# Optimization experiments

Measured on AMD Instinct MI355X. Metric: run time of the kernel, lower is better.

## Reference

```python
import jax, jax.numpy as jnp
import numpy as np

B, H, D, K, V, M = 64, 32, 4096, 128, 128, 4095

def setup_inputs() -> dict:
    key = jax.random.key(0)
    ks = jax.random.split(key, 7)
    return {
        "x": jax.random.normal(ks[0], (B, D), dtype=jnp.float32),
        "prev_K": jax.random.normal(ks[1], (B, M, K), dtype=jnp.float32),
        "prev_V": jax.random.normal(ks[2], (B, M, V), dtype=jnp.float32),
        "Wq": jax.random.normal(ks[3], (H, D, K), dtype=jnp.float32),
        "Wk": jax.random.normal(ks[4], (D, K), dtype=jnp.float32),
        "Wv": jax.random.normal(ks[5], (D, V), dtype=jnp.float32),
        "Wo": jax.random.normal(ks[6], (H, V, D), dtype=jnp.float32),
    }

def reference(x, prev_K, prev_V, Wq, Wk, Wv, Wo):
    # Projections
    q = jnp.einsum('bd,hdk->bhk', x, Wq)            # [b,h,k]
    k_new = jnp.einsum('bd,dk->bk', x, Wk)          # [b,k]
    v_new = jnp.einsum('bd,dv->bv', x, Wv)          # [b,v]
    Kc = jnp.concatenate([prev_K, k_new[:, None, :]], axis=1)  # [b,m+1,k]
    Vc = jnp.concatenate([prev_V, v_new[:, None, :]], axis=1)  # [b,m+1,v]
    # Shared-KV attention (MQA)
    logits = jnp.einsum('bhk,bmk->bhm', q, Kc)
    weights = jax.nn.softmax(logits, axis=-1)
    o = jnp.einsum('bhm,bmv->bhv', weights, Vc)
    y = jnp.einsum('bhv,hvd->bd', o, Wo)
    return (y, Kc, Vc)
```

## Files before the change

kernel.cpp:

```cpp
#include <hip/hip_runtime.h>
#include <stdint.h>

#define B_  64
#define H_  32
#define D_  4096
#define KD  128
#define VD  128
#define M_  4095
#define M1_ 4096
#define NCHUNK 32
#define LOG2E 1.44269504088896f

#define WS_P      0ull
#define WS_Q      4456448ull
#define WS_STATS  4718592ull
#define WS_O      4849664ull
#define WS_OPART  5111808ull

#define WAITVL(n) asm volatile("s_waitcnt vmcnt(" #n ") lgkmcnt(0)" ::: "memory")
#define WAITL()  asm volatile("s_waitcnt lgkmcnt(0)" ::: "memory")
#define BAR()    __builtin_amdgcn_s_barrier()

typedef __attribute__((address_space(3))) char lds_char;
typedef const __attribute__((address_space(1))) char glb_char;

__global__ __launch_bounds__(256) void k_proj_partial(
    const float* __restrict__ x, const float* __restrict__ Wq,
    const float* __restrict__ Wk, const float* __restrict__ Wv,
    float* __restrict__ P) {
  __shared__ float xs[64][260];
  const int dc = blockIdx.x;
  const int hx = blockIdx.y;
  const int t  = threadIdx.x;
  const float* xsrc = x + dc * 256;
  #pragma unroll
  for (int j = 0; j < 16; ++j) {
    int f = t + 256 * j;
    int row = f >> 6, c4 = f & 63;
    *(float4*)&xs[row][c4 * 4] =
        *(const float4*)(xsrc + (size_t)row * D_ + c4 * 4);
  }
  __syncthreads();
  const int bq = t >> 4;
  const int kg = t & 15;
  const int b0 = bq * 4;
  const float* W = (hx < H_) ? (Wq + (size_t)hx * D_ * KD)
                             : ((hx == H_) ? Wk : Wv);
  const float* wp = W + (size_t)(dc * 256) * KD + kg * 8;
  float acc[4][8];
  #pragma unroll
  for (int i = 0; i < 4; ++i)
    #pragma unroll
    for (int j = 0; j < 8; ++j) acc[i][j] = 0.f;
  #pragma unroll 8
  for (int d = 0; d < 256; ++d) {
    float4 w0 = *(const float4*)(wp + (size_t)d * KD);
    float4 w1 = *(const float4*)(wp + (size_t)d * KD + 4);
    float xv[4];
    #pragma unroll
    for (int i = 0; i < 4; ++i) xv[i] = xs[b0 + i][d];
    #pragma unroll
    for (int i = 0; i < 4; ++i) {
      acc[i][0] += xv[i] * w0.x; acc[i][1] += xv[i] * w0.y;
      acc[i][2] += xv[i] * w0.z; acc[i][3] += xv[i] * w0.w;
      acc[i][4] += xv[i] * w1.x; acc[i][5] += xv[i] * w1.y;
      acc[i][6] += xv[i] * w1.z; acc[i][7] += xv[i] * w1.w;
    }
  }
  #pragma unroll
  for (int i = 0; i < 4; ++i) {
    size_t base = ((size_t)(dc * 64 + b0 + i) * 34 + hx) * KD + kg * 8;
    *(float4*)&P[base]     = make_float4(acc[i][0], acc[i][1], acc[i][2], acc[i][3]);
    *(float4*)&P[base + 4] = make_float4(acc[i][4], acc[i][5], acc[i][6], acc[i][7]);
  }
}

__global__ __launch_bounds__(256) void k_proj_reduce(
    const float* __restrict__ P, float* __restrict__ q,
    float* __restrict__ Kc, float* __restrict__ Vc) {
  int i = blockIdx.x * 256 + threadIdx.x;
  int k = i & 127;
  int hx = (i >> 7) % 34;
  int b = i / (128 * 34);
  float s = 0.f;
  #pragma unroll
  for (int dc = 0; dc < 16; ++dc)
    s += P[(size_t)dc * (64 * 34 * 128) + (size_t)(b * 34 + hx) * 128 + k];
  if (hx < H_)       q[((size_t)b * H_ + hx) * KD + k] = s;
  else if (hx == H_) Kc[((size_t)b * M1_ + M_) * KD + k] = s;
  else               Vc[((size_t)b * M1_ + M_) * VD + k] = s;
}

__device__ __forceinline__ void stage_issue(
    const float* src, const float* app_row, float* lbuf, int m_lo, int t) {
  const int wb = t & ~63;
  #pragma unroll
  for (int j = 0; j < 4; ++j) {
    int f = j * 256 + t;
    int r = f >> 5, p = f & 31;
    int m = m_lo + r;
    int g4 = p ^ (r & 7);
    const float* gp = (m < M_) ? (src + (size_t)m * 128 + g4 * 4)
                               : (app_row + g4 * 4);
    __builtin_amdgcn_global_load_lds(
        (glb_char*)gp, (lds_char*)(lbuf + (size_t)(j * 256 + wb) * 4),
        16, 0, 0);
  }
}

__device__ __forceinline__ void copy_out(
    const float* lbuf, float* dst, int m_lo, int t) {
  const int r = t >> 3;
  const int m = m_lo + r;
  float* drow = dst + (size_t)m * 128;
  #pragma unroll
  for (int jj = 0; jj < 4; ++jj) {
    int g4 = (t & 7) + jj * 8;
    int p = g4 ^ (r & 7);
    float4 v = *(const float4*)&lbuf[(r * 32 + p) * 4];
    *(float4*)(drow + g4 * 4) = v;
  }
}

__global__ __launch_bounds__(256, 3) void k_flash(
    const float* __restrict__ prevK, const float* __restrict__ prevV,
    const float* __restrict__ q, float* __restrict__ Kc, float* __restrict__ Vc,
    float* __restrict__ o_part, float* __restrict__ stats) {
  __shared__ float buf[2][32 * 128];
  __shared__ float upool[4608];
  const int chunk = blockIdx.x;
  const int b = blockIdx.y;
  const int t = threadIdx.x;
  const int m0 = chunk * 128;

  const float* kbase = prevK + (size_t)b * M_ * KD;
  const float* vbase = prevV + (size_t)b * M_ * VD;
  const float* kapp  = Kc + ((size_t)b * M1_ + M_) * KD;
  const float* vapp  = Vc + ((size_t)b * M1_ + M_) * VD;
  float* kc = Kc + (size_t)b * M1_ * KD;
  float* vc = Vc + (size_t)b * M1_ * VD;

  const float* qsrc = q + (size_t)b * H_ * KD;
  float4 qv4[4];
  #pragma unroll
  for (int j = 0; j < 4; ++j) {
    int f = j * 256 + t;
    qv4[j] = *(const float4*)(qsrc + (size_t)(f >> 5) * KD + (f & 31) * 4);
  }
  stage_issue(kbase, kapp, buf[0], m0, t);
  #pragma unroll
  for (int j = 0; j < 4; ++j) {
    int f = j * 256 + t;
    *(float4*)&upool[(f >> 5) * 132 + (f & 31) * 4] = qv4[j];
  }

  const int mg = t & 15, hg = t >> 4, h0 = hg * 2;
  const int v4 = t & 31, hoct = t >> 5, h0v = hoct * 4;

  float accL0[8], accL1[8];

#define LOGITS_TILE(S, BUFI)                                                  \
  {                                                                           \
    const float* lb = buf[BUFI];                                              \
    float c00 = 0.f, c01 = 0.f, c10 = 0.f, c11 = 0.f;                         \
    const int sw = (mg & 7);                                                  \
    _Pragma("unroll 4")                                                       \
    for (int k4 = 0; k4 < 32; ++k4) {                                         \
      int p = (k4 ^ sw) * 4;                                                  \
      float4 qa = *(const float4*)&upool[h0 * 132 + k4 * 4];                  \
      float4 qb = *(const float4*)&upool[(h0 + 1) * 132 + k4 * 4];            \
      float4 k0v = *(const float4*)&lb[mg * 128 + p];                         \
      float4 k1v = *(const float4*)&lb[(mg + 16) * 128 + p];                  \
      c00 += qa.x*k0v.x + qa.y*k0v.y + qa.z*k0v.z + qa.w*k0v.w;               \
      c01 += qa.x*k1v.x + qa.y*k1v.y + qa.z*k1v.z + qa.w*k1v.w;               \
      c10 += qb.x*k0v.x + qb.y*k0v.y + qb.z*k0v.z + qb.w*k0v.w;               \
      c11 += qb.x*k1v.x + qb.y*k1v.y + qb.z*k1v.z + qb.w*k1v.w;               \
    }                                                                         \
    accL0[(S) * 2]     = c00;                                                 \
    accL0[(S) * 2 + 1] = c01;                                                 \
    accL1[(S) * 2]     = c10;                                                 \
    accL1[(S) * 2 + 1] = c11;                                                 \
  }

#define PV_TILE(S, BUFI)                                                      \
  {                                                                           \
    const float* lb = buf[BUFI];                                              \
    _Pragma("unroll 4")                                                       \
    for (int mm = 0; mm < 32; ++mm) {                                         \
      int p = (v4 ^ (mm & 7)) * 4;                                            \
      float4 gv = *(const float4*)&lb[mm * 128 + p];                          \
      float4 w4 = *(const float4*)&upool[((S) * 32 + mm) * 36 + h0v];         \
      a0.x += w4.x*gv.x; a0.y += w4.x*gv.y; a0.z += w4.x*gv.z; a0.w += w4.x*gv.w; \
      a1.x += w4.y*gv.x; a1.y += w4.y*gv.y; a1.z += w4.y*gv.z; a1.w += w4.y*gv.w; \
      a2.x += w4.z*gv.x; a2.y += w4.z*gv.y; a2.z += w4.z*gv.z; a2.w += w4.z*gv.w; \
      a3.x += w4.w*gv.x; a3.y += w4.w*gv.y; a3.z += w4.w*gv.z; a3.w += w4.w*gv.w; \
    }                                                                         \
  }

  stage_issue(kbase, kapp, buf[1], m0 + 32, t);
  WAITVL(4); BAR();
  LOGITS_TILE(0, 0);
  copy_out(buf[0], kc, m0, t);
  WAITL(); BAR();

  stage_issue(kbase, kapp, buf[0], m0 + 64, t);
  WAITVL(8); BAR();
  LOGITS_TILE(1, 1);
  copy_out(buf[1], kc, m0 + 32, t);
  WAITL(); BAR();

  stage_issue(kbase, kapp, buf[1], m0 + 96, t);
  WAITVL(8); BAR();
  LOGITS_TILE(2, 0);
  copy_out(buf[0], kc, m0 + 64, t);
  WAITL(); BAR();

  stage_issue(vbase, vapp, buf[0], m0, t);
  WAITVL(8); BAR();
  LOGITS_TILE(3, 1);
  copy_out(buf[1], kc, m0 + 96, t);
  WAITL(); BAR();

  {
    float mx0 = -3.402823466e38f, mx1 = -3.402823466e38f;
    #pragma unroll
    for (int j = 0; j < 8; ++j) {
      mx0 = fmaxf(mx0, accL0[j]);
      mx1 = fmaxf(mx1, accL1[j]);
    }
    #pragma unroll
    for (int off = 1; off <= 8; off <<= 1) {
      mx0 = fmaxf(mx0, __shfl_xor(mx0, off));
      mx1 = fmaxf(mx1, __shfl_xor(mx1, off));
    }
    float s0 = 0.f, s1 = 0.f;
    #pragma unroll
    for (int j = 0; j < 8; ++j) {
      float e0 = exp2f((accL0[j] - mx0) * LOG2E); accL0[j] = e0; s0 += e0;
      float e1 = exp2f((accL1[j] - mx1) * LOG2E); accL1[j] = e1; s1 += e1;
    }
    #pragma unroll
    for (int off = 1; off <= 8; off <<= 1) {
      s0 += __shfl_xor(s0, off);
      s1 += __shfl_xor(s1, off);
    }
    #pragma unroll
    for (int s = 0; s < 4; ++s)
      #pragma unroll
      for (int i = 0; i < 2; ++i) {
        int m = s * 32 + mg + 16 * i;
        upool[m * 36 + h0]     = accL0[s * 2 + i];
        upool[m * 36 + h0 + 1] = accL1[s * 2 + i];
      }
    if (mg == 0) {
      size_t sb0 = (((size_t)b * H_ + h0) * NCHUNK + chunk) * 2;
      *(float2*)&stats[sb0] = make_float2(mx0, s0);
      size_t sb1 = (((size_t)b * H_ + h0 + 1) * NCHUNK + chunk) * 2;
      *(float2*)&stats[sb1] = make_float2(mx1, s1);
    }
  }
  WAITL(); BAR();

  float4 a0 = {0,0,0,0}, a1 = {0,0,0,0}, a2 = {0,0,0,0}, a3 = {0,0,0,0};

  stage_issue(vbase, vapp, buf[1], m0 + 32, t);
  WAITVL(10); BAR();
  PV_TILE(0, 0);
  copy_out(buf[0], vc, m0, t);
  WAITL(); BAR();

  stage_issue(vbase, vapp, buf[0], m0 + 64, t);
  WAITVL(8); BAR();
  PV_TILE(1, 1);
  copy_out(buf[1], vc, m0 + 32, t);
  WAITL(); BAR();

  stage_issue(vbase, vapp, buf[1], m0 + 96, t);
  WAITVL(8); BAR();
  PV_TILE(2, 0);
  copy_out(buf[0], vc, m0 + 64, t);
  WAITL(); BAR();

  WAITVL(4); BAR();
  PV_TILE(3, 1);
  copy_out(buf[1], vc, m0 + 96, t);

  size_t base = ((size_t)(chunk * B_ + b) * H_ + h0v) * VD + v4 * 4;
  *(float4*)&o_part[base]          = a0;
  *(float4*)&o_part[base + VD]     = a1;
  *(float4*)&o_part[base + 2 * VD] = a2;
  *(float4*)&o_part[base + 3 * VD] = a3;
#undef LOGITS_TILE
#undef PV_TILE
}

__global__ __launch_bounds__(128) void k_combine(
    const float* __restrict__ o_part, const float* __restrict__ stats,
    float* __restrict__ o) {
  const int bh = blockIdx.x;
  const int t = threadIdx.x;
  __shared__ float st[64];
  if (t < 64) st[t] = stats[(size_t)bh * 64 + t];
  __syncthreads();
  float M = -3.402823466e38f;
  #pragma unroll
  for (int c = 0; c < NCHUNK; ++c) M = fmaxf(M, st[2 * c]);
  float wc[NCHUNK];
  float denom = 0.f;
  #pragma unroll
  for (int c = 0; c < NCHUNK; ++c) {
    float e = exp2f((st[2 * c] - M) * LOG2E);
    wc[c] = e;
    denom += st[2 * c + 1] * e;
  }
  const float inv = 1.0f / denom;
  const int b = bh >> 5, h = bh & 31;
  float acc = 0.f;
  #pragma unroll 4
  for (int c = 0; c < NCHUNK; ++c)
    acc += wc[c] * o_part[((size_t)(c * B_ + b) * H_ + h) * VD + t];
  o[(size_t)bh * VD + t] = acc * inv;
}

__global__ __launch_bounds__(256) void k_out_partial(
    const float* __restrict__ o, const float* __restrict__ Wo,
    float* __restrict__ Py) {
  __shared__ float os[64][260];
  const int dc = blockIdx.x;
  const int hvc = blockIdx.y;
  const int t = threadIdx.x;
  #pragma unroll
  for (int j = 0; j < 16; ++j) {
    int f = t + 256 * j;
    int row = f >> 6, c4 = f & 63;
    *(float4*)&os[row][c4 * 4] =
        *(const float4*)(o + (size_t)row * 4096 + hvc * 256 + c4 * 4);
  }
  __syncthreads();
  const int bq = t >> 4, dg = t & 15;
  const int b0 = bq * 4;
  const float* wp = Wo + (size_t)(hvc * 256) * D_ + dc * 128 + dg * 8;
  float acc[4][8];
  #pragma unroll
  for (int i = 0; i < 4; ++i)
    #pragma unroll
    for (int j = 0; j < 8; ++j) acc[i][j] = 0.f;
  #pragma unroll 8
  for (int hv = 0; hv < 256; ++hv) {
    float4 w0 = *(const float4*)(wp + (size_t)hv * D_);
    float4 w1 = *(const float4*)(wp + (size_t)hv * D_ + 4);
    float ov[4];
    #pragma unroll
    for (int i = 0; i < 4; ++i) ov[i] = os[b0 + i][hv];
    #pragma unroll
    for (int i = 0; i < 4; ++i) {
      acc[i][0] += ov[i] * w0.x; acc[i][1] += ov[i] * w0.y;
      acc[i][2] += ov[i] * w0.z; acc[i][3] += ov[i] * w0.w;
      acc[i][4] += ov[i] * w1.x; acc[i][5] += ov[i] * w1.y;
      acc[i][6] += ov[i] * w1.z; acc[i][7] += ov[i] * w1.w;
    }
  }
  #pragma unroll
  for (int i = 0; i < 4; ++i) {
    size_t base = ((size_t)hvc * 64 + b0 + i) * 4096 + dc * 128 + dg * 8;
    *(float4*)&Py[base]     = make_float4(acc[i][0], acc[i][1], acc[i][2], acc[i][3]);
    *(float4*)&Py[base + 4] = make_float4(acc[i][4], acc[i][5], acc[i][6], acc[i][7]);
  }
}

__global__ __launch_bounds__(256) void k_yreduce(
    const float* __restrict__ Py, float* __restrict__ y) {
  int i = blockIdx.x * 256 + threadIdx.x;
  float s = 0.f;
  #pragma unroll
  for (int c = 0; c < 16; ++c) s += Py[(size_t)c * 262144 + i];
  y[i] = s;
}

extern "C" void kernel_launch(void* const* d_in, const int* in_sizes, int n_in,
                              void* d_out, int out_size, void* d_ws, size_t ws_size,
                              hipStream_t stream) {
  const float* x     = (const float*)d_in[0];
  const float* prevK = (const float*)d_in[1];
  const float* prevV = (const float*)d_in[2];
  const float* Wq    = (const float*)d_in[3];
  const float* Wk    = (const float*)d_in[4];
  const float* Wv    = (const float*)d_in[5];
  const float* Wo    = (const float*)d_in[6];

  float* y  = (float*)d_out;
  float* Kc = y + (size_t)B_ * D_;
  float* Vc = Kc + (size_t)B_ * M1_ * KD;

  float* ws     = (float*)d_ws;
  float* P      = ws + WS_P;
  float* q      = ws + WS_Q;
  float* stats  = ws + WS_STATS;
  float* o      = ws + WS_O;
  float* o_part = ws + WS_OPART;

  k_proj_partial<<<dim3(16, 34), 256, 0, stream>>>(x, Wq, Wk, Wv, P);
  k_proj_reduce<<<1088, 256, 0, stream>>>(P, q, Kc, Vc);
  k_flash<<<dim3(32, 64), 256, 0, stream>>>(prevK, prevV, q, Kc, Vc, o_part, stats);
  k_combine<<<2048, 128, 0, stream>>>(o_part, stats, o);
  k_out_partial<<<dim3(32, 16), 256, 0, stream>>>(o, Wo, P);
  k_yreduce<<<1024, 256, 0, stream>>>(P, y);
}
```

Baseline: 262.0 us.

## Read V directly from global in PV loop instead of LDS staging

The PV phase no longer stages V tiles through LDS with async loads and barriers. Each thread now reads V rows straight from global memory, and one wave group writes the Vc copy. The second K stage issue is moved earlier and the V prefetch during the logits phase is dropped. This is meant to cut barrier and LDS traffic, at the cost of redundant global reads across the 8 head groups and less latency hiding.

```diff
diff --git a/kernel.cpp b/kernel.cpp
--- a/kernel.cpp
+++ b/kernel.cpp
@@ -148,6 +148,7 @@
     qv4[j] = *(const float4*)(qsrc + (size_t)(f >> 5) * KD + (f & 31) * 4);
   }
   stage_issue(kbase, kapp, buf[0], m0, t);
+  stage_issue(kbase, kapp, buf[1], m0 + 32, t);
   #pragma unroll
   for (int j = 0; j < 4; ++j) {
     int f = j * 256 + t;
@@ -182,22 +183,6 @@
     accL1[(S) * 2 + 1] = c11;                                                 \
   }
 
-#define PV_TILE(S, BUFI)                                                      \
-  {                                                                           \
-    const float* lb = buf[BUFI];                                              \
-    _Pragma("unroll 4")                                                       \
-    for (int mm = 0; mm < 32; ++mm) {                                         \
-      int p = (v4 ^ (mm & 7)) * 4;                                            \
-      float4 gv = *(const float4*)&lb[mm * 128 + p];                          \
-      float4 w4 = *(const float4*)&upool[((S) * 32 + mm) * 36 + h0v];         \
-      a0.x += w4.x*gv.x; a0.y += w4.x*gv.y; a0.z += w4.x*gv.z; a0.w += w4.x*gv.w; \
-      a1.x += w4.y*gv.x; a1.y += w4.y*gv.y; a1.z += w4.y*gv.z; a1.w += w4.y*gv.w; \
-      a2.x += w4.z*gv.x; a2.y += w4.z*gv.y; a2.z += w4.z*gv.z; a2.w += w4.z*gv.w; \
-      a3.x += w4.w*gv.x; a3.y += w4.w*gv.y; a3.z += w4.w*gv.z; a3.w += w4.w*gv.w; \
-    }                                                                         \
-  }
-
-  stage_issue(kbase, kapp, buf[1], m0 + 32, t);
   WAITVL(4); BAR();
   LOGITS_TILE(0, 0);
   copy_out(buf[0], kc, m0, t);
@@ -213,10 +198,7 @@
   WAITVL(8); BAR();
   LOGITS_TILE(2, 0);
   copy_out(buf[0], kc, m0 + 64, t);
-  WAITL(); BAR();
-
-  stage_issue(vbase, vapp, buf[0], m0, t);
-  WAITVL(8); BAR();
+  WAITVL(4); BAR();
   LOGITS_TILE(3, 1);
   copy_out(buf[1], kc, m0 + 96, t);
   WAITL(); BAR();
@@ -261,37 +243,28 @@
   }
   WAITL(); BAR();
 
-  float4 a0 = {0,0,0,0}, a1 = {0,0,0,0}, a2 = {0,0,0,0}, a3 = {0,0,0,0};
-
-  stage_issue(vbase, vapp, buf[1], m0 + 32, t);
-  WAITVL(10); BAR();
-  PV_TILE(0, 0);
-  copy_out(buf[0], vc, m0, t);
-  WAITL(); BAR();
-
-  stage_issue(vbase, vapp, buf[0], m0 + 64, t);
-  WAITVL(8); BAR();
-  PV_TILE(1, 1);
-  copy_out(buf[1], vc, m0 + 32, t);
-  WAITL(); BAR();
-
-  stage_issue(vbase, vapp, buf[1], m0 + 96, t);
-  WAITVL(8); BAR();
-  PV_TILE(2, 0);
-  copy_out(buf[0], vc, m0 + 64, t);
-  WAITL(); BAR();
-
-  WAITVL(4); BAR();
-  PV_TILE(3, 1);
-  copy_out(buf[1], vc, m0 + 96, t);
-
-  size_t base = ((size_t)(chunk * B_ + b) * H_ + h0v) * VD + v4 * 4;
-  *(float4*)&o_part[base]          = a0;
-  *(float4*)&o_part[base + VD]     = a1;
-  *(float4*)&o_part[base + 2 * VD] = a2;
-  *(float4*)&o_part[base + 3 * VD] = a3;
+  {
+    float4 a0 = {0,0,0,0}, a1 = {0,0,0,0}, a2 = {0,0,0,0}, a3 = {0,0,0,0};
+    #pragma unroll 8
+    for (int mm = 0; mm < 128; ++mm) {
+      const int mv = m0 + mm;
+      const float* vrow = (mv < M_) ? (vbase + (size_t)mv * VD) : vapp;
+      float4 gv = *(const float4*)(vrow + v4 * 4);
+      if (hoct == 0 && mv < M_)
+        *(float4*)(vc + (size_t)mv * VD + v4 * 4) = gv;
+      float4 w4 = *(const float4*)&upool[mm * 36 + h0v];
+      a0.x += w4.x*gv.x; a0.y += w4.x*gv.y; a0.z += w4.x*gv.z; a0.w += w4.x*gv.w;
+      a1.x += w4.y*gv.x; a1.y += w4.y*gv.y; a1.z += w4.y*gv.z; a1.w += w4.y*gv.w;
+      a2.x += w4.z*gv.x; a2.y += w4.z*gv.y; a2.z += w4.z*gv.z; a2.w += w4.z*gv.w;
+      a3.x += w4.w*gv.x; a3.y += w4.w*gv.y; a3.z += w4.w*gv.z; a3.w += w4.w*gv.w;
+    }
+    size_t base = ((size_t)(chunk * B_ + b) * H_ + h0v) * VD + v4 * 4;
+    *(float4*)&o_part[base]          = a0;
+    *(float4*)&o_part[base + VD]     = a1;
+    *(float4*)&o_part[base + 2 * VD] = a2;
+    *(float4*)&o_part[base + 3 * VD] = a3;
+  }
 #undef LOGITS_TILE
-#undef PV_TILE
 }
 
 __global__ __launch_bounds__(128) void k_combine(
```

Result: slower. 358.0 us (+36.6%).
